# Optimization experiments

Measured on AMD Instinct MI355X. Metric: run time of the kernel, lower is better.

## Reference

```python
import jax, jax.numpy as jnp
import numpy as np

N_CLUSTERS = 10

def _conv(x, w, b, stride):
    y = jax.lax.conv_general_dilated(x, w, stride, 'VALID', dimension_numbers=('NCHW', 'OIHW', 'NCHW'))
    return y + b[None, :, None, None]

def _forward(x, conv1_w, conv1_b, conv2_w, conv2_b, conv3_w, conv3_b,
             anc0_w, anc0_b, anc1_w, anc1_b, anc2_w, anc2_b, anc3_w, anc3_b,
             W1_w, W1_b, U_w, U_b, V_w, V_b, Wa_w, Wa_b,
             cluster_w, cluster_b, cls_w, cls_b):
    # backbone: three stride-2 valid convs
    h1 = _conv(x, conv1_w, conv1_b, (2, 2))
    h2 = _conv(h1, conv2_w, conv2_b, (2, 2))
    h3 = _conv(h2, conv3_w, conv3_b, (2, 2))  # [1,512,63,63]
    ancs = [_conv(h3, anc0_w, anc0_b, (1, 1)),
            _conv(h3, anc1_w, anc1_b, (1, 1)),
            _conv(h3, anc2_w, anc2_b, (1, 1)),
            _conv(h3, anc3_w, anc3_b, (1, 1))]
    ksizes = [(3, 3), (1, 1), (3, 1), (1, 3)]
    Hf, Wf = h3.shape[2], h3.shape[3]
    feats, coords = [], []
    # feat_organizer: flatten each anchor map to [Ha*Wa, 1024] and build normalized box coords
    for a, (kh, kw) in zip(ancs, ksizes):
        C, Ha, Wa = a.shape[1], a.shape[2], a.shape[3]
        feats.append(a[0].reshape(C, Ha * Wa).T)
        ys, xs = jnp.meshgrid(jnp.arange(Ha, dtype=jnp.float32), jnp.arange(Wa, dtype=jnp.float32), indexing='ij')
        cx = (xs.reshape(-1) + kw * 0.5) / Wf
        cy = (ys.reshape(-1) + kh * 0.5) / Hf
        bw = jnp.full((Ha * Wa,), kw / Wf, jnp.float32)
        bh = jnp.full((Ha * Wa,), kh / Hf, jnp.float32)
        coords.append(jnp.stack([cx, cy, bw, bh], axis=1))
    feat = jnp.concatenate(feats, 0)      # [N,1024]
    coords = jnp.concatenate(coords, 0)   # [N,4]
    # gated-attention MLP (AttentionHead)
    hmid = jax.nn.relu(feat @ W1_w.T + W1_b)              # [N,512]
    u = jax.nn.sigmoid(hmid @ U_w.T + U_b)                # [N,256]
    v = jnp.tanh(hmid @ V_w.T + V_b)                      # [N,256]
    att = jax.nn.sigmoid((u * v) @ Wa_w.T + Wa_b)[:, 0]   # [N]
    # cluster_features: rank anchors by attention, split into equal clusters,
    # attention-weighted segment reduce of features and box coords per cluster
    N = att.shape[0]
    rank = jnp.argsort(jnp.argsort(-att))
    cid = (rank * N_CLUSTERS) // N                         # [N] int cluster ids
    sw = jax.ops.segment_sum(att, cid, num_segments=N_CLUSTERS)                       # [nc]
    fc = jax.ops.segment_sum(hmid * att[:, None], cid, num_segments=N_CLUSTERS) / (sw[:, None] + 1e-8)   # [nc,512]
    pc = jax.ops.segment_sum(coords * att[:, None], cid, num_segments=N_CLUSTERS) / (sw[:, None] + 1e-8) # [nc,4]
    # ClusterAttention: conv with kernel (1,512) == per-cluster dot product, softmax over clusters
    scores = fc @ cluster_w + cluster_b                    # [nc]
    att_c = jax.nn.softmax(scores)
    # attention_pooling: attention-weighted sum of cluster features
    final = (att_c[:, None] * fc).sum(0, keepdims=True)    # [1,512]
    logits = final @ cls_w.T + cls_b
    return jax.nn.softmax(logits, axis=1), att_c.reshape(1, N_CLUSTERS, 1), pc

def setup_inputs() -> dict:
    key = jax.random.key(0)
    ks = jax.random.split(key, 30)
    def rn(k, shape, scale=0.02):
        return jax.random.normal(k, shape, jnp.float32) * scale
    d = {}
    d['x'] = jax.random.normal(ks[0], (1, 3, 512, 512), jnp.float32)
    d['conv1_w'] = rn(ks[1], (128, 3, 3, 3));    d['conv1_b'] = jnp.zeros((128,), jnp.float32)
    d['conv2_w'] = rn(ks[2], (256, 128, 3, 3));  d['conv2_b'] = jnp.zeros((256,), jnp.float32)
    d['conv3_w'] = rn(ks[3], (512, 256, 3, 3));  d['conv3_b'] = jnp.zeros((512,), jnp.float32)
    d['anc0_w'] = rn(ks[4], (1024, 512, 3, 3));  d['anc0_b'] = jnp.zeros((1024,), jnp.float32)
    d['anc1_w'] = rn(ks[5], (1024, 512, 1, 1));  d['anc1_b'] = jnp.zeros((1024,), jnp.float32)
    d['anc2_w'] = rn(ks[6], (1024, 512, 3, 1));  d['anc2_b'] = jnp.zeros((1024,), jnp.float32)
    d['anc3_w'] = rn(ks[7], (1024, 512, 1, 3));  d['anc3_b'] = jnp.zeros((1024,), jnp.float32)
    d['W1_w'] = rn(ks[8], (512, 1024));          d['W1_b'] = jnp.zeros((512,), jnp.float32)
    d['U_w'] = rn(ks[9], (256, 512));            d['U_b'] = jnp.zeros((256,), jnp.float32)
    d['V_w'] = rn(ks[10], (256, 512));           d['V_b'] = jnp.zeros((256,), jnp.float32)
    d['Wa_w'] = rn(ks[11], (1, 256));            d['Wa_b'] = jnp.zeros((1,), jnp.float32)
    d['cluster_w'] = rn(ks[12], (512,));         d['cluster_b'] = jnp.zeros((), jnp.float32)
    d['cls_w'] = rn(ks[13], (10, 512));          d['cls_b'] = jnp.zeros((10,), jnp.float32)
    return d

def reference(x, conv1_w, conv1_b, conv2_w, conv2_b, conv3_w, conv3_b,
              anc0_w, anc0_b, anc1_w, anc1_b, anc2_w, anc2_b, anc3_w, anc3_b,
              W1_w, W1_b, U_w, U_b, V_w, V_b, Wa_w, Wa_b,
              cluster_w, cluster_b, cls_w, cls_b):
    return _forward(x, conv1_w, conv1_b, conv2_w, conv2_b, conv3_w, conv3_b,
                    anc0_w, anc0_b, anc1_w, anc1_b, anc2_w, anc2_b, anc3_w, anc3_b,
                    W1_w, W1_b, U_w, U_b, V_w, V_b, Wa_w, Wa_b,
                    cluster_w, cluster_b, cls_w, cls_b)
```

## Files before the change

### kernel.cpp

```cpp
#include <hip/hip_runtime.h>
#include <math.h>


#define NTOT 15376
#define PHALF 2032128
typedef unsigned short u16;
typedef unsigned long long u64;
typedef __attribute__((ext_vector_type(8))) short bf16x8;
typedef __attribute__((ext_vector_type(4))) float f32x4;

static __device__ __forceinline__ u16 f2bf(float x) {
    union { float f; unsigned u; } v; v.f = x;
    unsigned r = v.u + 0x7FFF + ((v.u >> 16) & 1);
    return (u16)(r >> 16);
}
static __device__ __forceinline__ float bf2f(u16 h) {
    union { unsigned u; float f; } v; v.u = ((unsigned)h) << 16;
    return v.f;
}

static __device__ __forceinline__ void glds16(const void* g, void* l) {
    __builtin_amdgcn_global_load_lds(
        (const __attribute__((address_space(1))) void*)g,
        (__attribute__((address_space(3))) void*)l,
        16, 0, 0);
}

__global__ __launch_bounds__(256) void conv1k(
    const float* __restrict__ in, const float* __restrict__ wt,
    const float* __restrict__ bs, u16* __restrict__ h1T)
{
    int sp = blockIdx.x * 256 + threadIdx.x;
    if (sp >= 255 * 255) return;
    int oc0 = blockIdx.y * 16;
    int oy = sp / 255, ox = sp - oy * 255;
    const float* ip = in + (long)oy * 2 * 512 + ox * 2;
    float acc[16];
#pragma unroll
    for (int o = 0; o < 16; ++o) acc[o] = bs[oc0 + o];
#pragma unroll
    for (int ic = 0; ic < 3; ++ic)
#pragma unroll
        for (int ky = 0; ky < 3; ++ky)
#pragma unroll
            for (int kx = 0; kx < 3; ++kx) {
                float x = ip[ic * 262144 + ky * 512 + kx];
                const float* wp = wt + oc0 * 27 + ic * 9 + ky * 3 + kx;
#pragma unroll
                for (int o = 0; o < 16; ++o)
                    acc[o] = fmaf(x, wp[o * 27], acc[o]);
            }
    u16* dst = h1T + (long)sp * 128 + oc0;
#pragma unroll
    for (int g = 0; g < 4; ++g) {
        u64 pk = (u64)f2bf(acc[g * 4 + 0])
               | ((u64)f2bf(acc[g * 4 + 1]) << 16)
               | ((u64)f2bf(acc[g * 4 + 2]) << 32)
               | ((u64)f2bf(acc[g * 4 + 3]) << 48);
        *(u64*)(dst + g * 4) = pk;
    }
}

__global__ __launch_bounds__(256) void pack_all(
    const float* __restrict__ s0, const float* __restrict__ s1,
    const float* __restrict__ s2, const float* __restrict__ s3,
    const float* __restrict__ s4, const float* __restrict__ s5,
    const float* __restrict__ s6, const float* __restrict__ s7,
    const float* __restrict__ s8, u16* __restrict__ dst)
{
    long i = (long)blockIdx.x * 256 + threadIdx.x;
    if (i >= 10649600L) return;
    const long c1 = 4718592L, c2 = 5242880L, c3 = 6815744L, c4 = 8388608L,
               c5 = 8912896L, c7 = 9175040L, c8 = 9469952L;
    if (i >= c5 && i < c7) {
        long loc = i - c5;
        int ic = (int)(loc % 512);
        long row = loc / 512;
        const float* src = (row & 1) ? s6 : s5;
        long j = row >> 1;
        dst[i] = f2bf(src[j * 512 + ic]);
        return;
    }
    const float* src; long base; int IC, NT;
    if      (i < c1) { src = s0; base = 0;  IC = 512;  NT = 9; }
    else if (i < c2) { src = s1; base = c1; IC = 512;  NT = 1; }
    else if (i < c3) { src = s2; base = c2; IC = 512;  NT = 3; }
    else if (i < c4) { src = s3; base = c3; IC = 512;  NT = 3; }
    else if (i < c5) { src = s4; base = c4; IC = 1024; NT = 1; }
    else if (i < c8) { src = s7; base = c7; IC = 128;  NT = 9; }
    else             { src = s8; base = c8; IC = 256;  NT = 9; }
    long loc = i - base;
    int ic = (int)(loc % IC);
    long r = loc / IC;
    int t = (int)(r % NT);
    long oc = r / NT;
    dst[i] = f2bf(src[(oc * IC + ic) * NT + t]);
}

__global__ __launch_bounds__(256) void transp_w(
    const u16* __restrict__ Wpk, u16* __restrict__ WpkT)
{
    __shared__ u16 tile[64][65];
    int bid = blockIdx.x;
    int ocb = bid & 15;
    int rt  = bid >> 4;
    int kbase, rowlen; long sbase;
    if      (rt < 72)  { kbase = 0;    sbase = 0L;       rowlen = 4608; }
    else if (rt < 80)  { kbase = 4608; sbase = 4718592L; rowlen = 512;  }
    else if (rt < 104) { kbase = 5120; sbase = 5242880L; rowlen = 1536; }
    else               { kbase = 6656; sbase = 6815744L; rowlen = 1536; }
    int kloc0 = rt * 64 - kbase;
    int t = threadIdx.x, q = t >> 6, ln = t & 63;
#pragma unroll
    for (int i = 0; i < 16; ++i) {
        int ocl = q * 16 + i;
        tile[ocl][ln] = Wpk[sbase + (long)(ocb * 64 + ocl) * rowlen + kloc0 + ln];
    }
    __syncthreads();
#pragma unroll
    for (int i = 0; i < 16; ++i) {
        int kl = q * 16 + i;
        WpkT[(long)(rt * 64 + kl) * 1024 + ocb * 64 + ln] = tile[ln][kl];
    }
}

__global__ __launch_bounds__(256) void hbias_k(
    const float* __restrict__ W1w, const float* __restrict__ W1b,
    const float* __restrict__ b0, const float* __restrict__ b1,
    const float* __restrict__ b2, const float* __restrict__ b3,
    float* __restrict__ hb)
{
    int w = threadIdx.x >> 6, l = threadIdx.x & 63;
    int idx = blockIdx.x * 4 + w;
    int a = idx >> 9, m = idx & 511;
    const float* ab = (a == 0) ? b0 : (a == 1) ? b1 : (a == 2) ? b2 : b3;
    float s = 0.f;
    for (int j = l; j < 1024; j += 64)
        s = fmaf(W1w[(long)m * 1024 + j], ab[j], s);
#pragma unroll
    for (int d = 1; d < 64; d <<= 1) s += __shfl_xor(s, d, 64);
    if (l == 0) hb[idx] = s + W1b[m];
}

__global__ __launch_bounds__(256) void combA(
    const float* __restrict__ P, const float* __restrict__ hb,
    u16* __restrict__ Hfeat)
{
    int row = blockIdx.x;
    int oy = row / 61, ox = row - oy * 61;
    long n = (long)(oy * 63 + ox) * 512;
    int c = threadIdx.x * 2;
    float2 p0 = *(const float2*)(P + n + c);
    float2 p1 = *(const float2*)(P + PHALF + n + c);
    float2 b  = *(const float2*)(hb + c);
    unsigned pk = (unsigned)f2bf(fmaxf(p0.x + p1.x + b.x, 0.f))
                | ((unsigned)f2bf(fmaxf(p0.y + p1.y + b.y, 0.f)) << 16);
    *(unsigned*)(Hfeat + (long)row * 512 + c) = pk;
}

__global__ __launch_bounds__(256) void comb3(
    const float* __restrict__ P, const float* __restrict__ bias,
    u16* __restrict__ h3T)
{
    int row = blockIdx.x;
    int trg = (row / 63) * 65 + row % 63;
    long n = (long)row * 512;
    int c = threadIdx.x * 2;
    float2 q0 = *(const float2*)(P + n + c);
    float2 q1 = *(const float2*)(P + PHALF + n + c);
    float2 b  = *(const float2*)(bias + c);
    unsigned pk = (unsigned)f2bf(q0.x + q1.x + b.x)
                | ((unsigned)f2bf(q0.y + q1.y + b.y) << 16);
    *(unsigned*)(h3T + (long)trg * 512 + c) = pk;
}

template<int CMODE, int EMODE, int TMODE>
__global__ __launch_bounds__(256) void gemm_bt(
    const u16* __restrict__ A, const u16* __restrict__ B,
    const float* __restrict__ bias0, const float* __restrict__ bias1,
    const float* __restrict__ bias2, const float* __restrict__ bias3,
    void* __restrict__ Cout, float* __restrict__ Pbuf,
    int M, int N, int RSB, int Ktot, int OH, int OW, int obase)
{
    __shared__ u16 As[4096];
    __shared__ u16 Bs[8192];
    const int tid = threadIdx.x, w = tid >> 6, l = tid & 63;
    const int wr = w >> 1, wc = w & 1;
    const int sl = l & 7, sh = l >> 3, sx = sl ^ sh;

    int n0, m0;
    bool TW3 = false;
    int part = -1;
    int tbase = 0;
    const float* bias = bias0;
    constexpr int ICL2 = (TMODE == 5) ? 1 : (TMODE == 6) ? 2 : 3;
    constexpr int ICK  = 1 << ICL2;
    int ntaps;

    if (TMODE == 8) {
        int job = blockIdx.x >> 8, sub = blockIdx.x & 255;
        n0 = (sub & 31) * 128; m0 = (sub >> 5) * 64;
        int anc;
        if      (job == 0) { anc = 0; ntaps = 4; tbase = 0; part = 0; }
        else if (job == 1) { anc = 0; ntaps = 5; tbase = 4; part = 1; }
        else if (job == 2) { anc = 1; ntaps = 1; }
        else if (job == 3) { anc = 2; ntaps = 3; }
        else               { anc = 3; ntaps = 3; }
        TW3 = (anc == 0 || anc == 3);
        A += (anc == 0) ? 0 : (anc == 1) ? 4608 : (anc == 2) ? 5120 : 6656;
        obase = (anc == 0) ? 0 : (anc == 1) ? 3721 : (anc == 2) ? 7690 : 11533;
        OH = (anc == 0 || anc == 2) ? 61 : 63;
        OW = (anc == 0 || anc == 3) ? 61 : 63;
        bias = bias0 + anc * 512;
    } else if (TMODE == 6 && EMODE == 7) {
        int half = blockIdx.y >> 3;
        n0 = blockIdx.x * 128; m0 = (blockIdx.y & 7) * 64;
        ntaps = half ? 5 : 4; tbase = half * 4;
        Cout = (void*)((float*)Cout + (long)half * PHALF);
    } else {
        n0 = blockIdx.x * 128; m0 = blockIdx.y * 64;
        ntaps = Ktot >> ICL2;
    }
    const long RSA = (TMODE == 8) ? 8192 : (long)Ktot * 64;
    const long RSB2 = (long)RSB * 2;

    int offB[4], ldsOffB[4], ldsOffA[2];
    const char* aBase[2];
    const char* bBase[4];
#pragma unroll
    for (int j = 0; j < 4; ++j) {
        int r = w * 32 + j * 8 + sh;
        int gn = n0 + r;
        if (CMODE == 0)      { gn = min(gn, 3968);  offB[j] = (gn / 63) * 65 + (gn % 63); }
        else if (CMODE == 1) { offB[j] = min(gn, N - 1); }
        else if (CMODE == 2) { gn = min(gn, 16128); offB[j] = (gn / 127) * 510 + (gn % 127) * 2; }
        else                 { gn = min(gn, 3968);  offB[j] = (gn / 63) * 254 + (gn % 63) * 2; }
        ldsOffB[j] = r * 128;
        bBase[j] = (const char*)B + (long)offB[j] * RSB2 + sx * 16;
    }
#pragma unroll
    for (int j = 0; j < 2; ++j) {
        int r = w * 16 + j * 8 + sh;
        ldsOffA[j] = r * 128;
        aBase[j] = (const char*)A + (long)(m0 + r) * RSA * 2 + sx * 16;
    }

    f32x4 acc[2][4];
#pragma unroll
    for (int a = 0; a < 2; ++a)
#pragma unroll
        for (int b = 0; b < 4; ++b) acc[a][b] = (f32x4){0.f, 0.f, 0.f, 0.f};

    for (int t_ = 0; t_ < ntaps; ++t_) {
        int te = t_ + tbase;
        long tOffB;
        if (TMODE == 8) {
            int trow_;
            if (TW3) { int q_ = (te * 11) >> 5; trow_ = q_ * 65 + (te - q_ * 3); }
            else       trow_ = te * 65;
            tOffB = (long)trow_ * RSB2;
        } else if (TMODE == 4) {
            tOffB = (long)te * 1024;
        } else if (TMODE == 5) {
            int q_ = (te * 11) >> 5;
            tOffB = (long)(q_ * 255 + (te - q_ * 3)) * RSB2;
        } else if (TMODE == 6) {
            int q_ = (te * 11) >> 5;
            tOffB = (long)(q_ * 127 + (te - q_ * 3)) * RSB2;
        } else {
            tOffB = 0;
        }
        long aOff = (long)te * (ICK * 128);
#pragma unroll
        for (int kb = 0; kb < ICK; ++kb) {
#pragma unroll
            for (int j = 0; j < 2; ++j)
                glds16(aBase[j] + aOff + kb * 128, (char*)As + ldsOffA[j]);
#pragma unroll
            for (int j = 0; j < 4; ++j)
                glds16(bBase[j] + tOffB + kb * 128, (char*)Bs + ldsOffB[j]);
            __syncthreads();
#pragma unroll
            for (int kk = 0; kk < 2; ++kk) {
                bf16x8 af[2], bfr[4];
#pragma unroll
                for (int f = 0; f < 2; ++f) {
                    int rm = wr * 32 + f * 16 + (l & 15);
                    af[f] = *(const bf16x8*)((const char*)As + rm * 128 +
                               (((kk * 4 + (l >> 4)) ^ (rm & 7)) * 16));
                }
#pragma unroll
                for (int f = 0; f < 4; ++f) {
                    int rn = wc * 64 + f * 16 + (l & 15);
                    bfr[f] = *(const bf16x8*)((const char*)Bs + rn * 128 +
                               (((kk * 4 + (l >> 4)) ^ (rn & 7)) * 16));
                }
#pragma unroll
                for (int fm = 0; fm < 2; ++fm)
#pragma unroll
                    for (int fn = 0; fn < 4; ++fn)
                        acc[fm][fn] = __builtin_amdgcn_mfma_f32_16x16x32_bf16(
                            af[fm], bfr[fn], acc[fm][fn], 0, 0, 0);
            }
            __syncthreads();
        }
    }

#pragma unroll
    for (int fm = 0; fm < 2; ++fm) {
        int gmb = m0 + wr * 32 + fm * 16 + (l >> 4) * 4;
#pragma unroll
        for (int fn = 0; fn < 4; ++fn) {
            int gn = n0 + wc * 64 + fn * 16 + (l & 15);
            f32x4 v = acc[fm][fn];
            if (EMODE == 2) {
                if (gn < N) {
                    int j0 = gmb >> 1;
                    float u0 = 1.f / (1.f + expf(-(v.x + bias0[j0])));
                    float t0 = tanhf(v.y + bias1[j0]);
                    float u1 = 1.f / (1.f + expf(-(v.z + bias0[j0 + 1])));
                    float t1 = tanhf(v.w + bias1[j0 + 1]);
                    float2 o = { u0 * t0 * bias2[j0], u1 * t1 * bias2[j0 + 1] };
                    *(float2*)((float*)Cout + (long)gn * 256 + j0) = o;
                }
            } else if (EMODE == 4) {
                if (gn < N) {
                    float4 bv = *(const float4*)(bias + gmb);
                    u64 pk = (u64)f2bf(v.x + bv.x)
                           | ((u64)f2bf(v.y + bv.y) << 16)
                           | ((u64)f2bf(v.z + bv.z) << 32)
                           | ((u64)f2bf(v.w + bv.w) << 48);
                    *(u64*)((u16*)Cout + (long)gn * M + gmb) = pk;
                }
            } else if (EMODE == 5) {
                if (TMODE == 8 && part >= 0) {
                    if (gn < 3969) {
                        float4 o = { v.x, v.y, v.z, v.w };
                        *(float4*)(Pbuf + (long)part * PHALF + (long)gn * 512 + gmb) = o;
                    }
                } else if (gn < 3969) {
                    int oy = gn / 63, ox = gn - oy * 63;
                    if (oy < OH && ox < OW) {
                        int trg = obase + oy * OW + ox;
                        float4 bv = *(const float4*)(bias + gmb);
                        u64 pk = (u64)f2bf(fmaxf(v.x + bv.x, 0.f))
                               | ((u64)f2bf(fmaxf(v.y + bv.y, 0.f)) << 16)
                               | ((u64)f2bf(fmaxf(v.z + bv.z, 0.f)) << 32)
                               | ((u64)f2bf(fmaxf(v.w + bv.w, 0.f)) << 48);
                        *(u64*)((u16*)Cout + (long)trg * M + gmb) = pk;
                    }
                }
            } else if (EMODE == 6) {
                if (gn < N) {
                    u64 pk = (u64)f2bf(v.x)
                           | ((u64)f2bf(v.y) << 16)
                           | ((u64)f2bf(v.z) << 32)
                           | ((u64)f2bf(v.w) << 48);
                    *(u64*)((u16*)Cout + (long)gn * M + gmb) = pk;
                }
            } else {
                if (gn < 3969) {
                    float4 o = { v.x, v.y, v.z, v.w };
                    *(float4*)((float*)Cout + (long)gn * 512 + gmb) = o;
                }
            }
        }
    }
}

__global__ __launch_bounds__(256) void att_v3(
    const float* __restrict__ UVw, const float* __restrict__ Wab,
    float* __restrict__ att, int* __restrict__ rank, int N)
{
    int t = threadIdx.x, l = t & 63, r = t >> 6;
    int n = blockIdx.x * 4 + r;
    if (t < 4 && blockIdx.x * 4 + t < N) rank[blockIdx.x * 4 + t] = 0;
    if (n >= N) return;
    float4 p = *(const float4*)(UVw + (long)n * 256 + l * 4);
    float s = (p.x + p.y) + (p.z + p.w);
#pragma unroll
    for (int d = 1; d < 64; d <<= 1) s += __shfl_xor(s, d, 64);
    if (l == 0) att[n] = 1.f / (1.f + expf(-(s + Wab[0])));
}

__global__ __launch_bounds__(256) void rank_partial(
    const float* __restrict__ att, int* __restrict__ rank, int N)
{
    __shared__ float sa[1024];
    int n = blockIdx.x * 256 + threadIdx.x;
    int base = blockIdx.y * 1024;
    int cnt = min(1024, N - base);
    for (int t = threadIdx.x; t < cnt; t += 256) sa[t] = att[base + t];
    __syncthreads();
    if (n >= N) return;
    float a = att[n];
    int r = 0;
    for (int t = 0; t < cnt; ++t) {
        float aj = sa[t];
        int j = base + t;
        r += (int)(aj > a) | ((int)(aj == a) & (int)(j < n));
    }
    atomicAdd(&rank[n], r);
}

#define FC_NB 256
#define FC_ROWS 61
__global__ __launch_bounds__(256) void fc_part(
    const u16* __restrict__ Hfeat, const float* __restrict__ att,
    const int* __restrict__ rank, float* __restrict__ fcp, int N)
{
    int t = threadIdx.x, b = blockIdx.x;
    int l = t & 63, r = t >> 6;
    float acc[10][8];
#pragma unroll
    for (int k = 0; k < 10; ++k)
#pragma unroll
        for (int e = 0; e < 8; ++e) acc[k][e] = 0.f;
    int n0 = b * FC_ROWS;
    for (int it = 0; it < 16; ++it) {
        int nl = it * 4 + r;
        int n = n0 + nl;
        if (nl >= FC_ROWS || n >= N) break;
        float a = att[n];
        int c = (rank[n] * 10) / N;
        bf16x8 h8 = *(const bf16x8*)(Hfeat + (long)n * 512 + l * 8);
        float hf[8];
#pragma unroll
        for (int e = 0; e < 8; ++e) hf[e] = bf2f((u16)h8[e]);
#pragma unroll
        for (int k = 0; k < 10; ++k) {
            float sel = (c == k) ? a : 0.f;
#pragma unroll
            for (int e = 0; e < 8; ++e)
                acc[k][e] = fmaf(sel, hf[e], acc[k][e]);
        }
    }
    float* dst = fcp + (long)b * 5120 + l * 8;
#pragma unroll
    for (int k = 0; k < 10; ++k)
#pragma unroll
        for (int e = 0; e < 8; ++e) dst[k * 512 + e] = acc[k][e];
}

__global__ __launch_bounds__(256) void fc_sum(
    const float* __restrict__ fcp, float* __restrict__ fc_raw)
{
    int i = blockIdx.x * 256 + threadIdx.x;
    if (i >= 5120) return;
    float s = 0.f;
    for (int b = 0; b < FC_NB; ++b) s += fcp[(long)b * 5120 + i];
    fc_raw[i] = s;
}

__device__ __forceinline__ void anchor_coords(int n, float& cx, float& cy,
                                              float& bw, float& bh)
{
    int kh, kw, Wa, loc;
    if (n < 3721)       { kh = 3; kw = 3; Wa = 61; loc = n; }
    else if (n < 7690)  { kh = 1; kw = 1; Wa = 63; loc = n - 3721; }
    else if (n < 11533) { kh = 3; kw = 1; Wa = 63; loc = n - 7690; }
    else                { kh = 1; kw = 3; Wa = 61; loc = n - 11533; }
    int iy = loc / Wa, ix = loc - iy * Wa;
    cx = (ix + kw * 0.5f) * (1.f / 63.f);
    cy = (iy + kh * 0.5f) * (1.f / 63.f);
    bw = kw * (1.f / 63.f);
    bh = kh * (1.f / 63.f);
}

__global__ __launch_bounds__(256) void swpc_part(
    const float* __restrict__ att, const int* __restrict__ rank,
    float* __restrict__ prt, int N)
{
    __shared__ float red[4][50];
    int t = threadIdx.x, b = blockIdx.x;
    int n = b * 256 + t;
    int l = t & 63, w = t >> 6;
    float a = 0.f, cx = 0.f, cy = 0.f, bw = 0.f, bh = 0.f;
    int c = -1;
    if (n < N) {
        a = att[n]; c = (rank[n] * 10) / N;
        anchor_coords(n, cx, cy, bw, bh);
    }
#pragma unroll
    for (int k = 0; k < 10; ++k) {
        float sel = (c == k) ? a : 0.f;
        float v[5] = {sel, sel * cx, sel * cy, sel * bw, sel * bh};
#pragma unroll
        for (int d = 0; d < 5; ++d) {
            float x = v[d];
#pragma unroll
            for (int s = 1; s < 64; s <<= 1) x += __shfl_xor(x, s, 64);
            if (l == 0) red[w][k * 5 + d] = x;
        }
    }
    __syncthreads();
    if (t < 50) prt[b * 50 + t] = red[0][t] + red[1][t] + red[2][t] + red[3][t];
}

__global__ __launch_bounds__(512) void final_kernel(
    const float* __restrict__ fc_raw, const float* __restrict__ prt,
    const float* __restrict__ cluster_w, const float* __restrict__ cluster_b,
    const float* __restrict__ cls_w, const float* __restrict__ cls_b,
    float* __restrict__ out)
{
    __shared__ float red[512];
    __shared__ float swpc[50];
    int t = threadIdx.x;
    if (t < 50) {
        float s = 0.f;
        for (int b = 0; b < 61; ++b) s += prt[b * 50 + t];
        swpc[t] = s;
    }
    __syncthreads();
    float fcn[10];
#pragma unroll
    for (int k = 0; k < 10; ++k)
        fcn[k] = fc_raw[k * 512 + t] / (swpc[k * 5] + 1e-8f);
    float cw = cluster_w[t];
    float sc[10];
#pragma unroll
    for (int k = 0; k < 10; ++k) {
        red[t] = fcn[k] * cw;
        __syncthreads();
        for (int s = 256; s > 0; s >>= 1) {
            if (t < s) red[t] += red[t + s];
            __syncthreads();
        }
        sc[k] = red[0] + cluster_b[0];
        __syncthreads();
    }
    float mx = sc[0];
#pragma unroll
    for (int k = 1; k < 10; ++k) mx = fmaxf(mx, sc[k]);
    float se = 0.f;
#pragma unroll
    for (int k = 0; k < 10; ++k) { sc[k] = expf(sc[k] - mx); se += sc[k]; }
    float inv = 1.f / se;
#pragma unroll
    for (int k = 0; k < 10; ++k) sc[k] *= inv;
    float fm = 0.f;
#pragma unroll
    for (int k = 0; k < 10; ++k) fm = fmaf(sc[k], fcn[k], fm);
    float lg[10];
#pragma unroll
    for (int c = 0; c < 10; ++c) {
        red[t] = fm * cls_w[c * 512 + t];
        __syncthreads();
        for (int s = 256; s > 0; s >>= 1) {
            if (t < s) red[t] += red[t + s];
            __syncthreads();
        }
        lg[c] = red[0] + cls_b[c];
        __syncthreads();
    }
    float mx2 = lg[0];
#pragma unroll
    for (int c = 1; c < 10; ++c) mx2 = fmaxf(mx2, lg[c]);
    float se2 = 0.f;
#pragma unroll
    for (int c = 0; c < 10; ++c) { lg[c] = expf(lg[c] - mx2); se2 += lg[c]; }
    float inv2 = 1.f / se2;
    if (t < 10) out[t] = lg[t] * inv2;
    if (t >= 10 && t < 20) out[t] = sc[t - 10];
    if (t >= 20 && t < 60) {
        int i = t - 20;
        int k = i >> 2, d = i & 3;
        out[t] = swpc[k * 5 + 1 + d] / (swpc[k * 5] + 1e-8f);
    }
}

extern "C" void kernel_launch(void* const* d_in, const int* in_sizes, int n_in,
                              void* d_out, int out_size, void* d_ws, size_t ws_size,
                              hipStream_t stream)
{
    const float* x    = (const float*)d_in[0];
    const float* c1w  = (const float*)d_in[1];   const float* c1b = (const float*)d_in[2];
    const float* c2w  = (const float*)d_in[3];   const float* c2b = (const float*)d_in[4];
    const float* c3w  = (const float*)d_in[5];   const float* c3b = (const float*)d_in[6];
    const float* a0w  = (const float*)d_in[7];   const float* a0b = (const float*)d_in[8];
    const float* a1w  = (const float*)d_in[9];   const float* a1b = (const float*)d_in[10];
    const float* a2w  = (const float*)d_in[11];  const float* a2b = (const float*)d_in[12];
    const float* a3w  = (const float*)d_in[13];  const float* a3b = (const float*)d_in[14];
    const float* W1w  = (const float*)d_in[15];  const float* W1b = (const float*)d_in[16];
    const float* Uw   = (const float*)d_in[17];  const float* Ub  = (const float*)d_in[18];
    const float* Vw   = (const float*)d_in[19];  const float* Vb  = (const float*)d_in[20];
    const float* Waw  = (const float*)d_in[21];  const float* Wab = (const float*)d_in[22];
    const float* clw  = (const float*)d_in[23];  const float* clb = (const float*)d_in[24];
    const float* clsw = (const float*)d_in[25];  const float* clsb= (const float*)d_in[26];
    float* out = (float*)d_out;

    float* ws = (float*)d_ws;
    u16*   Hfeat= (u16*)ws;
    u16*   h1T  = (u16*)(ws + 3936256);
    float* P    = ws + 3936256;
    u16*   h2T  = (u16*)(ws + 8097856);
    u16*   h3T  = (u16*)(ws + 10162368);
    float* UVw  = ws + 11243968;
    u16*   Wpk  = (u16*)(ws + 15180224);
    u16*   WpkT = (u16*)(ws + 20505024);
    u16*   WcAll= (u16*)(ws + 24699328);
    float* hb   = ws + 26796480;
    float* att  = ws + 26798528;
    int*   rank = (int*)(ws + 26813904);
    float* fcr  = ws + 26829280;
    float* fcp  = ws + 26834400;
    float* prt  = ws + 28145120;

    u16* W1pk  = Wpk + 8388608;
    u16* UVpk  = Wpk + 8912896;
    u16* Wc2pk = Wpk + 9175040;
    u16* Wc3pk = Wpk + 9469952;

    dim3 blk(256);
    const float* nul = nullptr;
    float* fnul = nullptr;

    pack_all<<<dim3(41600), blk, 0, stream>>>(a0w, a1w, a2w, a3w, W1w, Uw, Vw,
                                              c2w, c3w, Wpk);
    transp_w<<<dim3(2048), blk, 0, stream>>>(Wpk, WpkT);
    gemm_bt<1,6,4><<<dim3(4, 128), blk, 0, stream>>>(WpkT, W1pk, nul, nul, nul, nul, WcAll, fnul, 8192, 512, 1024, 16, 0, 0, 0);
    hbias_k<<<dim3(512), blk, 0, stream>>>(W1w, W1b, a0b, a1b, a2b, a3b, hb);

    conv1k<<<dim3(255, 8), blk, 0, stream>>>(x, c1w, c1b, h1T);
    gemm_bt<2,4,5><<<dim3(127, 4), blk, 0, stream>>>(Wc2pk, h1T, c2b, nul, nul, nul, h2T, fnul, 256, 16129, 128, 18, 0, 0, 0);
    gemm_bt<3,7,6><<<dim3(32, 16), blk, 0, stream>>>(Wc3pk, h2T, nul, nul, nul, nul, P, fnul, 512, 3969, 256, 36, 0, 0, 0);
    comb3<<<dim3(3969), blk, 0, stream>>>(P, c3b, h3T);

    gemm_bt<0,5,8><<<dim3(1280), blk, 0, stream>>>(WcAll, h3T, hb, nul, nul, nul, Hfeat, P, 512, 3969, 512, 0, 0, 0, 0);
    combA<<<dim3(3721), blk, 0, stream>>>(P, hb, Hfeat);

    gemm_bt<1,2,1><<<dim3(121, 8), blk, 0, stream>>>(UVpk, Hfeat, Ub, Vb, Waw, nul, UVw, fnul, 512, NTOT, 512, 8, 0, 0, 0);

    att_v3<<<dim3(3844), blk, 0, stream>>>(UVw, Wab, att, rank, NTOT);
    rank_partial<<<dim3(61, 16), blk, 0, stream>>>(att, rank, NTOT);
    fc_part<<<dim3(FC_NB), blk, 0, stream>>>(Hfeat, att, rank, fcp, NTOT);
    fc_sum<<<dim3(20), blk, 0, stream>>>(fcp, fcr);
    swpc_part<<<dim3(61), blk, 0, stream>>>(att, rank, prt, NTOT);
    final_kernel<<<dim3(1), dim3(512), 0, stream>>>(fcr, prt, clw, clb, clsw, clsb, out);
}
```

Before: 313.5 us.

## Move conv1 to MFMA GEMM via im2col, merge prep and tail kernels, split anchor0 taps

Conv1 is no longer a scalar FMA kernel. It becomes an im2col bf16 pack (K padded to 64) in a merged prep kernel, followed by a gemm_bt instantiation with a new TMODE 9. The weight pack, UV pack, conv1 weight pack, im2col and hbias are merged into one launch, and fc_part and swpc_part are merged into one tail kernel to cut launches. The anchor-0 GEMM is split into four tap partitions instead of two to give more blocks, which means combA now sums four partial buffers and P moves to a larger workspace region. The trade-offs are extra im2col memory traffic and partial-sum bandwidth, plus bf16 rounding of the input image.

```diff
diff --git a/kernel.cpp b/kernel.cpp
--- a/kernel.cpp
+++ b/kernel.cpp
@@ -26,75 +26,89 @@
         16, 0, 0);
 }
 
-__global__ __launch_bounds__(256) void conv1k(
-    const float* __restrict__ in, const float* __restrict__ wt,
-    const float* __restrict__ bs, u16* __restrict__ h1T)
-{
-    int sp = blockIdx.x * 256 + threadIdx.x;
-    if (sp >= 255 * 255) return;
-    int oc0 = blockIdx.y * 16;
-    int oy = sp / 255, ox = sp - oy * 255;
-    const float* ip = in + (long)oy * 2 * 512 + ox * 2;
-    float acc[16];
-#pragma unroll
-    for (int o = 0; o < 16; ++o) acc[o] = bs[oc0 + o];
-#pragma unroll
-    for (int ic = 0; ic < 3; ++ic)
-#pragma unroll
-        for (int ky = 0; ky < 3; ++ky)
-#pragma unroll
-            for (int kx = 0; kx < 3; ++kx) {
-                float x = ip[ic * 262144 + ky * 512 + kx];
-                const float* wp = wt + oc0 * 27 + ic * 9 + ky * 3 + kx;
-#pragma unroll
-                for (int o = 0; o < 16; ++o)
-                    acc[o] = fmaf(x, wp[o * 27], acc[o]);
-            }
-    u16* dst = h1T + (long)sp * 128 + oc0;
-#pragma unroll
-    for (int g = 0; g < 4; ++g) {
-        u64 pk = (u64)f2bf(acc[g * 4 + 0])
-               | ((u64)f2bf(acc[g * 4 + 1]) << 16)
-               | ((u64)f2bf(acc[g * 4 + 2]) << 32)
-               | ((u64)f2bf(acc[g * 4 + 3]) << 48);
-        *(u64*)(dst + g * 4) = pk;
-    }
-}
-
-__global__ __launch_bounds__(256) void pack_all(
+__global__ __launch_bounds__(256) void prep_all(
     const float* __restrict__ s0, const float* __restrict__ s1,
     const float* __restrict__ s2, const float* __restrict__ s3,
     const float* __restrict__ s4, const float* __restrict__ s5,
     const float* __restrict__ s6, const float* __restrict__ s7,
-    const float* __restrict__ s8, u16* __restrict__ dst)
-{
-    long i = (long)blockIdx.x * 256 + threadIdx.x;
-    if (i >= 10649600L) return;
-    const long c1 = 4718592L, c2 = 5242880L, c3 = 6815744L, c4 = 8388608L,
-               c5 = 8912896L, c7 = 9175040L, c8 = 9469952L;
-    if (i >= c5 && i < c7) {
-        long loc = i - c5;
-        int ic = (int)(loc % 512);
-        long row = loc / 512;
-        const float* src = (row & 1) ? s6 : s5;
-        long j = row >> 1;
-        dst[i] = f2bf(src[j * 512 + ic]);
-        return;
-    }
-    const float* src; long base; int IC, NT;
-    if      (i < c1) { src = s0; base = 0;  IC = 512;  NT = 9; }
-    else if (i < c2) { src = s1; base = c1; IC = 512;  NT = 1; }
-    else if (i < c3) { src = s2; base = c2; IC = 512;  NT = 3; }
-    else if (i < c4) { src = s3; base = c3; IC = 512;  NT = 3; }
-    else if (i < c5) { src = s4; base = c4; IC = 1024; NT = 1; }
-    else if (i < c8) { src = s7; base = c7; IC = 128;  NT = 9; }
-    else             { src = s8; base = c8; IC = 256;  NT = 9; }
-    long loc = i - base;
-    int ic = (int)(loc % IC);
-    long r = loc / IC;
-    int t = (int)(r % NT);
-    long oc = r / NT;
-    dst[i] = f2bf(src[(oc * IC + ic) * NT + t]);
+    const float* __restrict__ s8, u16* __restrict__ dst,
+    u16* __restrict__ UVsep,
+    const float* __restrict__ c1w, u16* __restrict__ Wc1pk,
+    const float* __restrict__ x, u16* __restrict__ x_t,
+    const float* __restrict__ W1w, const float* __restrict__ W1b,
+    const float* __restrict__ b0, const float* __restrict__ b1,
+    const float* __restrict__ b2, const float* __restrict__ b3,
+    float* __restrict__ hb)
+{
+    int b = blockIdx.x, t = threadIdx.x;
+    if (b < 41600) {
+        long i = (long)b * 256 + t;
+        if (i >= 10649600L) return;
+        const long c1 = 4718592L, c2 = 5242880L, c3 = 6815744L, c4 = 8388608L,
+                   c5 = 8912896L, c7 = 9175040L, c8 = 9469952L;
+        if (i >= c5 && i < c7) {
+            long loc = i - c5;
+            int ic = (int)(loc % 512);
+            long row = loc / 512;
+            const float* src = (row & 1) ? s6 : s5;
+            long j = row >> 1;
+            UVsep[loc] = f2bf(src[j * 512 + ic]);
+            return;
+        }
+        const float* src; long base; int IC, NT;
+        if      (i < c1) { src = s0; base = 0;  IC = 512;  NT = 9; }
+        else if (i < c2) { src = s1; base = c1; IC = 512;  NT = 1; }
+        else if (i < c3) { src = s2; base = c2; IC = 512;  NT = 3; }
+        else if (i < c4) { src = s3; base = c3; IC = 512;  NT = 3; }
+        else if (i < c5) { src = s4; base = c4; IC = 1024; NT = 1; }
+        else if (i < c8) { src = s7; base = c7; IC = 128;  NT = 9; }
+        else             { src = s8; base = c8; IC = 256;  NT = 9; }
+        long loc = i - base;
+        int ic = (int)(loc % IC);
+        long r = loc / IC;
+        int tt = (int)(r % NT);
+        long oc = r / NT;
+        dst[i] = f2bf(src[(oc * IC + ic) * NT + tt]);
+    } else if (b < 41632) {
+        int j = (b - 41600) * 256 + t;
+        if (j < 8192) {
+            int oc = j >> 6, k = j & 63;
+            Wc1pk[j] = (k < 27) ? f2bf(c1w[oc * 27 + k]) : (u16)0;
+        }
+    } else if (b < 41887) {
+        int sp = (b - 41632) * 256 + t;
+        if (sp < 65025) {
+            int oy = sp / 255, ox = sp - oy * 255;
+            const float* base = x + (long)oy * 2 * 512 + ox * 2;
+            u64 pk[16];
+#pragma unroll
+            for (int q = 0; q < 16; ++q) pk[q] = 0;
+#pragma unroll
+            for (int ic = 0; ic < 3; ++ic)
+#pragma unroll
+                for (int ky = 0; ky < 3; ++ky)
+#pragma unroll
+                    for (int kx = 0; kx < 3; ++kx) {
+                        int k = ic * 9 + ky * 3 + kx;
+                        float v = base[ic * 262144 + ky * 512 + kx];
+                        pk[k >> 2] |= (u64)f2bf(v) << ((k & 3) * 16);
+                    }
+            u64* drow = (u64*)(x_t + (long)sp * 64);
+#pragma unroll
+            for (int q = 0; q < 16; ++q) drow[q] = pk[q];
+        }
+    } else {
+        int w = t >> 6, l = t & 63;
+        int idx = (b - 41887) * 4 + w;
+        int a = idx >> 9, m = idx & 511;
+        const float* ab = (a == 0) ? b0 : (a == 1) ? b1 : (a == 2) ? b2 : b3;
+        float s = 0.f;
+        for (int j = l; j < 1024; j += 64)
+            s = fmaf(W1w[(long)m * 1024 + j], ab[j], s);
+#pragma unroll
+        for (int d = 1; d < 64; d <<= 1) s += __shfl_xor(s, d, 64);
+        if (l == 0) hb[idx] = s + W1b[m];
+    }
 }
 
 __global__ __launch_bounds__(256) void transp_w(
@@ -124,24 +138,6 @@
     }
 }
 
-__global__ __launch_bounds__(256) void hbias_k(
-    const float* __restrict__ W1w, const float* __restrict__ W1b,
-    const float* __restrict__ b0, const float* __restrict__ b1,
-    const float* __restrict__ b2, const float* __restrict__ b3,
-    float* __restrict__ hb)
-{
-    int w = threadIdx.x >> 6, l = threadIdx.x & 63;
-    int idx = blockIdx.x * 4 + w;
-    int a = idx >> 9, m = idx & 511;
-    const float* ab = (a == 0) ? b0 : (a == 1) ? b1 : (a == 2) ? b2 : b3;
-    float s = 0.f;
-    for (int j = l; j < 1024; j += 64)
-        s = fmaf(W1w[(long)m * 1024 + j], ab[j], s);
-#pragma unroll
-    for (int d = 1; d < 64; d <<= 1) s += __shfl_xor(s, d, 64);
-    if (l == 0) hb[idx] = s + W1b[m];
-}
-
 __global__ __launch_bounds__(256) void combA(
     const float* __restrict__ P, const float* __restrict__ hb,
     u16* __restrict__ Hfeat)
@@ -152,9 +148,13 @@
     int c = threadIdx.x * 2;
     float2 p0 = *(const float2*)(P + n + c);
     float2 p1 = *(const float2*)(P + PHALF + n + c);
-    float2 b  = *(const float2*)(hb + c);
-    unsigned pk = (unsigned)f2bf(fmaxf(p0.x + p1.x + b.x, 0.f))
-                | ((unsigned)f2bf(fmaxf(p0.y + p1.y + b.y, 0.f)) << 16);
+    float2 p2 = *(const float2*)(P + 2L * PHALF + n + c);
+    float2 p3 = *(const float2*)(P + 3L * PHALF + n + c);
+    float2 bv = *(const float2*)(hb + c);
+    float sx = ((p0.x + p1.x) + (p2.x + p3.x)) + bv.x;
+    float sy = ((p0.y + p1.y) + (p2.y + p3.y)) + bv.y;
+    unsigned pk = (unsigned)f2bf(fmaxf(sx, 0.f))
+                | ((unsigned)f2bf(fmaxf(sy, 0.f)) << 16);
     *(unsigned*)(Hfeat + (long)row * 512 + c) = pk;
 }
 
@@ -193,7 +193,7 @@
     int part = -1;
     int tbase = 0;
     const float* bias = bias0;
-    constexpr int ICL2 = (TMODE == 5) ? 1 : (TMODE == 6) ? 2 : 3;
+    constexpr int ICL2 = (TMODE == 5) ? 1 : (TMODE == 6) ? 2 : (TMODE == 9) ? 0 : 3;
     constexpr int ICK  = 1 << ICL2;
     int ntaps;
 
@@ -201,10 +201,12 @@
         int job = blockIdx.x >> 8, sub = blockIdx.x & 255;
         n0 = (sub & 31) * 128; m0 = (sub >> 5) * 64;
         int anc;
-        if      (job == 0) { anc = 0; ntaps = 4; tbase = 0; part = 0; }
-        else if (job == 1) { anc = 0; ntaps = 5; tbase = 4; part = 1; }
-        else if (job == 2) { anc = 1; ntaps = 1; }
-        else if (job == 3) { anc = 2; ntaps = 3; }
+        if      (job == 0) { anc = 0; ntaps = 3; tbase = 0; part = 0; }
+        else if (job == 1) { anc = 0; ntaps = 2; tbase = 3; part = 1; }
+        else if (job == 2) { anc = 0; ntaps = 2; tbase = 5; part = 2; }
+        else if (job == 3) { anc = 0; ntaps = 2; tbase = 7; part = 3; }
+        else if (job == 4) { anc = 1; ntaps = 1; }
+        else if (job == 5) { anc = 2; ntaps = 3; }
         else               { anc = 3; ntaps = 3; }
         TW3 = (anc == 0 || anc == 3);
         A += (anc == 0) ? 0 : (anc == 1) ? 4608 : (anc == 2) ? 5120 : 6656;
@@ -405,53 +407,6 @@
 
 #define FC_NB 256
 #define FC_ROWS 61
-__global__ __launch_bounds__(256) void fc_part(
-    const u16* __restrict__ Hfeat, const float* __restrict__ att,
-    const int* __restrict__ rank, float* __restrict__ fcp, int N)
-{
-    int t = threadIdx.x, b = blockIdx.x;
-    int l = t & 63, r = t >> 6;
-    float acc[10][8];
-#pragma unroll
-    for (int k = 0; k < 10; ++k)
-#pragma unroll
-        for (int e = 0; e < 8; ++e) acc[k][e] = 0.f;
-    int n0 = b * FC_ROWS;
-    for (int it = 0; it < 16; ++it) {
-        int nl = it * 4 + r;
-        int n = n0 + nl;
-        if (nl >= FC_ROWS || n >= N) break;
-        float a = att[n];
-        int c = (rank[n] * 10) / N;
-        bf16x8 h8 = *(const bf16x8*)(Hfeat + (long)n * 512 + l * 8);
-        float hf[8];
-#pragma unroll
-        for (int e = 0; e < 8; ++e) hf[e] = bf2f((u16)h8[e]);
-#pragma unroll
-        for (int k = 0; k < 10; ++k) {
-            float sel = (c == k) ? a : 0.f;
-#pragma unroll
-            for (int e = 0; e < 8; ++e)
-                acc[k][e] = fmaf(sel, hf[e], acc[k][e]);
-        }
-    }
-    float* dst = fcp + (long)b * 5120 + l * 8;
-#pragma unroll
-    for (int k = 0; k < 10; ++k)
-#pragma unroll
-        for (int e = 0; e < 8; ++e) dst[k * 512 + e] = acc[k][e];
-}
-
-__global__ __launch_bounds__(256) void fc_sum(
-    const float* __restrict__ fcp, float* __restrict__ fc_raw)
-{
-    int i = blockIdx.x * 256 + threadIdx.x;
-    if (i >= 5120) return;
-    float s = 0.f;
-    for (int b = 0; b < FC_NB; ++b) s += fcp[(long)b * 5120 + i];
-    fc_raw[i] = s;
-}
-
 __device__ __forceinline__ void anchor_coords(int n, float& cx, float& cy,
                                               float& bw, float& bh)
 {
@@ -467,34 +422,80 @@
     bh = kh * (1.f / 63.f);
 }
 
-__global__ __launch_bounds__(256) void swpc_part(
-    const float* __restrict__ att, const int* __restrict__ rank,
+__global__ __launch_bounds__(256) void tail_part(
+    const u16* __restrict__ Hfeat, const float* __restrict__ att,
+    const int* __restrict__ rank, float* __restrict__ fcp,
     float* __restrict__ prt, int N)
 {
     __shared__ float red[4][50];
-    int t = threadIdx.x, b = blockIdx.x;
-    int n = b * 256 + t;
-    int l = t & 63, w = t >> 6;
-    float a = 0.f, cx = 0.f, cy = 0.f, bw = 0.f, bh = 0.f;
-    int c = -1;
-    if (n < N) {
-        a = att[n]; c = (rank[n] * 10) / N;
-        anchor_coords(n, cx, cy, bw, bh);
-    }
-#pragma unroll
-    for (int k = 0; k < 10; ++k) {
-        float sel = (c == k) ? a : 0.f;
-        float v[5] = {sel, sel * cx, sel * cy, sel * bw, sel * bh};
-#pragma unroll
-        for (int d = 0; d < 5; ++d) {
-            float x = v[d];
-#pragma unroll
-            for (int s = 1; s < 64; s <<= 1) x += __shfl_xor(x, s, 64);
-            if (l == 0) red[w][k * 5 + d] = x;
-        }
-    }
-    __syncthreads();
-    if (t < 50) prt[b * 50 + t] = red[0][t] + red[1][t] + red[2][t] + red[3][t];
+    int t = threadIdx.x;
+    if (blockIdx.x < FC_NB) {
+        int b = blockIdx.x;
+        int l = t & 63, r = t >> 6;
+        float acc[10][8];
+#pragma unroll
+        for (int k = 0; k < 10; ++k)
+#pragma unroll
+            for (int e = 0; e < 8; ++e) acc[k][e] = 0.f;
+        int n0 = b * FC_ROWS;
+        for (int it = 0; it < 16; ++it) {
+            int nl = it * 4 + r;
+            int n = n0 + nl;
+            if (nl >= FC_ROWS || n >= N) break;
+            float a = att[n];
+            int c = (rank[n] * 10) / N;
+            bf16x8 h8 = *(const bf16x8*)(Hfeat + (long)n * 512 + l * 8);
+            float hf[8];
+#pragma unroll
+            for (int e = 0; e < 8; ++e) hf[e] = bf2f((u16)h8[e]);
+#pragma unroll
+            for (int k = 0; k < 10; ++k) {
+                float sel = (c == k) ? a : 0.f;
+#pragma unroll
+                for (int e = 0; e < 8; ++e)
+                    acc[k][e] = fmaf(sel, hf[e], acc[k][e]);
+            }
+        }
+        float* dst = fcp + (long)b * 5120 + l * 8;
+#pragma unroll
+        for (int k = 0; k < 10; ++k)
+#pragma unroll
+            for (int e = 0; e < 8; ++e) dst[k * 512 + e] = acc[k][e];
+    } else {
+        int b = blockIdx.x - FC_NB;
+        int n = b * 256 + t;
+        int l = t & 63, w = t >> 6;
+        float a = 0.f, cx = 0.f, cy = 0.f, bw = 0.f, bh = 0.f;
+        int c = -1;
+        if (n < N) {
+            a = att[n]; c = (rank[n] * 10) / N;
+            anchor_coords(n, cx, cy, bw, bh);
+        }
+#pragma unroll
+        for (int k = 0; k < 10; ++k) {
+            float sel = (c == k) ? a : 0.f;
+            float v[5] = {sel, sel * cx, sel * cy, sel * bw, sel * bh};
+#pragma unroll
+            for (int d = 0; d < 5; ++d) {
+                float x = v[d];
+#pragma unroll
+                for (int s = 1; s < 64; s <<= 1) x += __shfl_xor(x, s, 64);
+                if (l == 0) red[w][k * 5 + d] = x;
+            }
+        }
+        __syncthreads();
+        if (t < 50) prt[b * 50 + t] = red[0][t] + red[1][t] + red[2][t] + red[3][t];
+    }
+}
+
+__global__ __launch_bounds__(256) void fc_sum(
+    const float* __restrict__ fcp, float* __restrict__ fc_raw)
+{
+    int i = blockIdx.x * 256 + threadIdx.x;
+    if (i >= 5120) return;
+    float s = 0.f;
+    for (int b = 0; b < FC_NB; ++b) s += fcp[(long)b * 5120 + i];
+    fc_raw[i] = s;
 }
 
 __global__ __launch_bounds__(512) void final_kernel(
@@ -592,11 +593,12 @@
     float* ws = (float*)d_ws;
     u16*   Hfeat= (u16*)ws;
     u16*   h1T  = (u16*)(ws + 3936256);
-    float* P    = ws + 3936256;
     u16*   h2T  = (u16*)(ws + 8097856);
     u16*   h3T  = (u16*)(ws + 10162368);
     float* UVw  = ws + 11243968;
+    u16*   x_t  = (u16*)(ws + 11243968);
     u16*   Wpk  = (u16*)(ws + 15180224);
+    float* P    = ws + 15180224;
     u16*   WpkT = (u16*)(ws + 20505024);
     u16*   WcAll= (u16*)(ws + 24699328);
     float* hb   = ws + 26796480;
@@ -605,9 +607,10 @@
     float* fcr  = ws + 26829280;
     float* fcp  = ws + 26834400;
     float* prt  = ws + 28145120;
+    u16*   Wc1pk= (u16*)(ws + 28148224);
+    u16*   UVpk = (u16*)(ws + 28152320);
 
     u16* W1pk  = Wpk + 8388608;
-    u16* UVpk  = Wpk + 8912896;
     u16* Wc2pk = Wpk + 9175040;
     u16* Wc3pk = Wpk + 9469952;
 
@@ -615,26 +618,28 @@
     const float* nul = nullptr;
     float* fnul = nullptr;
 
-    pack_all<<<dim3(41600), blk, 0, stream>>>(a0w, a1w, a2w, a3w, W1w, Uw, Vw,
-                                              c2w, c3w, Wpk);
+    prep_all<<<dim3(42399), blk, 0, stream>>>(a0w, a1w, a2w, a3w, W1w, Uw, Vw,
+                                              c2w, c3w, Wpk, UVpk, c1w, Wc1pk,
+                                              x, x_t, W1w, W1b, a0b, a1b, a2b,
+                                              a3b, hb);
+
+    gemm_bt<1,4,9><<<dim3(509, 2), blk, 0, stream>>>(Wc1pk, x_t, c1b, nul, nul, nul, h1T, fnul, 128, 65025, 64, 1, 0, 0, 0);
+
     transp_w<<<dim3(2048), blk, 0, stream>>>(Wpk, WpkT);
     gemm_bt<1,6,4><<<dim3(4, 128), blk, 0, stream>>>(WpkT, W1pk, nul, nul, nul, nul, WcAll, fnul, 8192, 512, 1024, 16, 0, 0, 0);
-    hbias_k<<<dim3(512), blk, 0, stream>>>(W1w, W1b, a0b, a1b, a2b, a3b, hb);
-
-    conv1k<<<dim3(255, 8), blk, 0, stream>>>(x, c1w, c1b, h1T);
+
     gemm_bt<2,4,5><<<dim3(127, 4), blk, 0, stream>>>(Wc2pk, h1T, c2b, nul, nul, nul, h2T, fnul, 256, 16129, 128, 18, 0, 0, 0);
     gemm_bt<3,7,6><<<dim3(32, 16), blk, 0, stream>>>(Wc3pk, h2T, nul, nul, nul, nul, P, fnul, 512, 3969, 256, 36, 0, 0, 0);
     comb3<<<dim3(3969), blk, 0, stream>>>(P, c3b, h3T);
 
-    gemm_bt<0,5,8><<<dim3(1280), blk, 0, stream>>>(WcAll, h3T, hb, nul, nul, nul, Hfeat, P, 512, 3969, 512, 0, 0, 0, 0);
+    gemm_bt<0,5,8><<<dim3(1792), blk, 0, stream>>>(WcAll, h3T, hb, nul, nul, nul, Hfeat, P, 512, 3969, 512, 0, 0, 0, 0);
     combA<<<dim3(3721), blk, 0, stream>>>(P, hb, Hfeat);
 
     gemm_bt<1,2,1><<<dim3(121, 8), blk, 0, stream>>>(UVpk, Hfeat, Ub, Vb, Waw, nul, UVw, fnul, 512, NTOT, 512, 8, 0, 0, 0);
 
     att_v3<<<dim3(3844), blk, 0, stream>>>(UVw, Wab, att, rank, NTOT);
     rank_partial<<<dim3(61, 16), blk, 0, stream>>>(att, rank, NTOT);
-    fc_part<<<dim3(FC_NB), blk, 0, stream>>>(Hfeat, att, rank, fcp, NTOT);
+    tail_part<<<dim3(FC_NB + 61), blk, 0, stream>>>(Hfeat, att, rank, fcp, prt, NTOT);
     fc_sum<<<dim3(20), blk, 0, stream>>>(fcp, fcr);
-    swpc_part<<<dim3(61), blk, 0, stream>>>(att, rank, prt, NTOT);
     final_kernel<<<dim3(1), dim3(512), 0, stream>>>(fcr, prt, clw, clb, clsw, clsb, out);
 }
```

New measurement: 302.8 us. 3.4% less time.
